# Kernel tuning notes

Measured on AMD Instinct MI355X. Metric: run time of the kernel, lower is better.

Reference implementation:

```python
import jax, jax.numpy as jnp
import numpy as np

NEG = -1.0e4  # finite stand-in for log(0) of the zero initial state (exp(NEG)==0 in fp32)


def log_g(x):
    # log of g(x) = where(x>=0, x+0.5, sigmoid(x))
    return jnp.where(x >= 0, jnp.log(jax.nn.relu(x) + 0.5), -jax.nn.softplus(-x))


def setup_inputs() -> dict:
    key = jax.random.key(0)
    k1, k2, k3 = jax.random.split(key, 3)
    B, S, D, H, O = 8, 8192, 512, 512, 512
    x = jax.random.normal(k1, (B, S, D), dtype=jnp.float32)
    is_init = jnp.zeros((B,), dtype=bool)  # unused in training mode (h_0 is None)
    W_hg = jax.random.normal(k2, (2 * H, D), dtype=jnp.float32) / np.float32(np.sqrt(D))
    W_out = jax.random.normal(k3, (O, H), dtype=jnp.float32) / np.float32(np.sqrt(H))
    return {"x": x, "is_init": is_init, "W_hg": W_hg, "W_out": W_out}


def reference(x, is_init, W_hg, W_out):
    B, S, _ = x.shape
    H = W_hg.shape[0] // 2
    hg = jnp.einsum('bsd,ed->bse', x, W_hg)          # [B,S,2H]
    hidden, gate = hg[..., :H], hg[..., H:]
    log_coeffs = -jax.nn.softplus(gate)              # log(1 - z)
    log_values = -jax.nn.softplus(-gate) + log_g(hidden)  # log z + log g(h~)
    # prepend h_0 = 0 -> log(h_0) ~ NEG; pad coeffs with a leading 0
    log_values = jnp.concatenate(
        [jnp.full((B, 1, H), NEG, dtype=x.dtype), log_values], axis=1)
    log_coeffs = jnp.pad(log_coeffs, ((0, 0), (1, 0), (0, 0)))
    # Heinsen log-space associative scan
    a_star = jnp.cumsum(log_coeffs, axis=1)
    log_h = a_star + jax.lax.cumlogsumexp(log_values - a_star, axis=1)
    h = jnp.exp(log_h)[:, 1:]                        # drop the h_0 slot -> [B,S,H]
    h_n = h[:, -1:]                                  # [B,1,H]
    out = jnp.einsum('bsh,oh->bso', h, W_out)        # [B,S,O]
    return (out, h_n)
```

## Files before the change

kernel.cpp:

```cpp
#include <hip/hip_runtime.h>
#include <stdint.h>

typedef __bf16 bf16;
typedef bf16 bf16x8 __attribute__((ext_vector_type(8)));
typedef bf16 bf16x4 __attribute__((ext_vector_type(4)));
typedef float f32x4 __attribute__((ext_vector_type(4)));

#define MFMA16(a, b, c) __builtin_amdgcn_mfma_f32_16x16x32_bf16(a, b, c, 0, 0, 0)

__device__ __forceinline__ void gll16(const void* g, void* l) {
    __builtin_amdgcn_global_load_lds(
        (const __attribute__((address_space(1))) void*)g,
        (__attribute__((address_space(3))) void*)l, 16, 0, 0);
}

__device__ __forceinline__ float frcp(float x) { return __builtin_amdgcn_rcpf(x); }

__device__ __forceinline__ float bflo(uint32_t u) {
    union { uint32_t i; float f; } x; x.i = u << 16; return x.f;
}
__device__ __forceinline__ float bfhi(uint32_t u) {
    union { uint32_t i; float f; } x; x.i = u & 0xffff0000u; return x.f;
}
__device__ __forceinline__ uint32_t packcv(float c, float v) {
    union { bf16 b[2]; uint32_t u; } p;
    p.b[0] = (bf16)c; p.b[1] = (bf16)v; return p.u;
}

__global__ __launch_bounds__(256) void conv_kernel(
    const float* __restrict__ X, const float* __restrict__ Whg,
    const float* __restrict__ Wout, bf16* __restrict__ Xbf,
    bf16* __restrict__ Whg_bf, bf16* __restrict__ Wout_bf) {
    int i = blockIdx.x * 256 + threadIdx.x;
    if (i < 8388608) {
        f32x4 v = ((const f32x4*)X)[i];
        ((bf16x4*)Xbf)[i] = __builtin_convertvector(v, bf16x4);
    } else if (i < 8388608 + 131072) {
        int j = i - 8388608;
        f32x4 v = ((const f32x4*)Whg)[j];
        ((bf16x4*)Whg_bf)[j] = __builtin_convertvector(v, bf16x4);
    } else {
        int j = i - (8388608 + 131072);
        f32x4 v = ((const f32x4*)Wout)[j];
        ((bf16x4*)Wout_bf)[j] = __builtin_convertvector(v, bf16x4);
    }
}

__global__ __launch_bounds__(256) void gemm1_kernel(
    const bf16* __restrict__ Xbf, const bf16* __restrict__ W,
    uint32_t* __restrict__ CV) {
    constexpr int K = 512;
    __shared__ bf16 As[128 * 64];
    __shared__ bf16 Bh[128 * 64];
    __shared__ bf16 Bg[128 * 64];

    const int t = threadIdx.x;
    const size_t m0 = (size_t)blockIdx.x * 128;
    const int n0 = blockIdx.y * 128;
    const int w = t >> 6, lane = t & 63;
    const int wm = (w >> 1) * 64, wn = (w & 1) * 64;
    const int r16 = lane & 15, quad = lane >> 4;
    const int sw = r16 & 7;

    f32x4 ah[4][4] = {};
    f32x4 ag[4][4] = {};

    for (int k0 = 0; k0 < K; k0 += 64) {
        __syncthreads();
        #pragma unroll
        for (int r = 0; r < 4; ++r) {
            int g = r * 256 + t;
            int row = g >> 3;
            int c8 = (g & 7) ^ (row & 7);
            gll16(Xbf + (m0 + row) * K + k0 + c8 * 8, &As[g * 8]);
            gll16(W + (size_t)(n0 + row) * K + k0 + c8 * 8, &Bh[g * 8]);
            gll16(W + (size_t)(512 + n0 + row) * K + k0 + c8 * 8, &Bg[g * 8]);
        }
        __syncthreads();
        #pragma unroll
        for (int kk = 0; kk < 2; ++kk) {
            const int kg = kk * 4 + quad;
            bf16x8 af[4], bhf[4], bgf[4];
            #pragma unroll
            for (int i = 0; i < 4; ++i) {
                int arow = wm + i * 16 + r16;
                af[i] = *(const bf16x8*)&As[arow * 64 + (kg ^ sw) * 8];
            }
            #pragma unroll
            for (int i = 0; i < 4; ++i) {
                int brow = wn + i * 16 + r16;
                bhf[i] = *(const bf16x8*)&Bh[brow * 64 + (kg ^ sw) * 8];
                bgf[i] = *(const bf16x8*)&Bg[brow * 64 + (kg ^ sw) * 8];
            }
            #pragma unroll
            for (int mi = 0; mi < 4; ++mi)
                #pragma unroll
                for (int ni = 0; ni < 4; ++ni) {
                    ah[mi][ni] = MFMA16(af[mi], bhf[ni], ah[mi][ni]);
                    ag[mi][ni] = MFMA16(af[mi], bgf[ni], ag[mi][ni]);
                }
        }
    }
    #pragma unroll
    for (int mi = 0; mi < 4; ++mi)
        #pragma unroll
        for (int ni = 0; ni < 4; ++ni)
            #pragma unroll
            for (int r = 0; r < 4; ++r) {
                size_t row = m0 + wm + mi * 16 + quad * 4 + r;
                int col = n0 + wn + ni * 16 + r16;
                float hid = ah[mi][ni][r], gat = ag[mi][ni][r];
                float z = frcp(1.f + __expf(-gat));
                float c = 1.f - z;
                float gv = hid >= 0.f ? hid + 0.5f : frcp(1.f + __expf(-hid));
                CV[row * 512 + col] = packcv(c, z * gv);
            }
}

#define NC 64
#define CHUNK 128

__global__ __launch_bounds__(256) void scan1_kernel(
    const uint32_t* __restrict__ CV, float2* __restrict__ agg) {
    int idx = blockIdx.x * 256 + threadIdx.x;
    int h = idx & 511;
    int ch = (idx >> 9) & (NC - 1);
    int b = idx >> 15;
    const uint32_t* p = CV + (((size_t)b * 8192 + (size_t)ch * CHUNK) * 512 + h);
    float C = 1.f, V = 0.f;
    for (int tt = 0; tt < CHUNK; tt += 8) {
        uint32_t u[8];
        #pragma unroll
        for (int j = 0; j < 8; ++j) u[j] = p[(size_t)(tt + j) * 512];
        #pragma unroll
        for (int j = 0; j < 8; ++j) {
            float c = bflo(u[j]), v = bfhi(u[j]);
            C *= c;
            V = c * V + v;
        }
    }
    agg[idx] = make_float2(C, V);
}

__global__ __launch_bounds__(256) void scan2_kernel(
    const float2* __restrict__ agg, float* __restrict__ h0) {
    int idx = blockIdx.x * 256 + threadIdx.x;
    int h = idx & 511;
    int b = idx >> 9;
    float hr = 0.f;
    for (int ch = 0; ch < NC; ++ch) {
        size_t o = ((size_t)b * NC + ch) * 512 + h;
        h0[o] = hr;
        float2 a = agg[o];
        hr = a.x * hr + a.y;
    }
}

__global__ __launch_bounds__(256) void scan3_kernel(
    const uint32_t* __restrict__ CV, const float* __restrict__ h0,
    bf16* __restrict__ Hbf, float* __restrict__ hn) {
    int idx = blockIdx.x * 256 + threadIdx.x;
    int h = idx & 511;
    int ch = (idx >> 9) & (NC - 1);
    int b = idx >> 15;
    size_t base = ((size_t)b * 8192 + (size_t)ch * CHUNK) * 512 + h;
    const uint32_t* p = CV + base;
    bf16* q = Hbf + base;
    float hcur = h0[idx];
    for (int tt = 0; tt < CHUNK; tt += 8) {
        uint32_t u[8];
        #pragma unroll
        for (int j = 0; j < 8; ++j) u[j] = p[(size_t)(tt + j) * 512];
        #pragma unroll
        for (int j = 0; j < 8; ++j) {
            float c = bflo(u[j]), v = bfhi(u[j]);
            hcur = c * hcur + v;
            q[(size_t)(tt + j) * 512] = (bf16)hcur;
        }
    }
    if (ch == NC - 1) hn[b * 512 + h] = hcur;
}

__global__ __launch_bounds__(256) void gemm2_kernel(
    const bf16* __restrict__ Ah, const bf16* __restrict__ Wo,
    float* __restrict__ Out) {
    constexpr int K = 512;
    __shared__ bf16 As[128 * 64];
    __shared__ bf16 Bs[128 * 64];
    const int t = threadIdx.x;
    const size_t m0 = (size_t)blockIdx.x * 128;
    const int n0 = blockIdx.y * 128;
    const int w = t >> 6, lane = t & 63;
    const int wm = (w >> 1) * 64, wn = (w & 1) * 64;
    const int r16 = lane & 15, quad = lane >> 4;
    const int sw = r16 & 7;
    f32x4 acc[4][4] = {};
    for (int k0 = 0; k0 < K; k0 += 64) {
        __syncthreads();
        #pragma unroll
        for (int r = 0; r < 4; ++r) {
            int g = r * 256 + t;
            int row = g >> 3;
            int c8 = (g & 7) ^ (row & 7);
            gll16(Ah + (m0 + row) * K + k0 + c8 * 8, &As[g * 8]);
            gll16(Wo + (size_t)(n0 + row) * K + k0 + c8 * 8, &Bs[g * 8]);
        }
        __syncthreads();
        #pragma unroll
        for (int kk = 0; kk < 2; ++kk) {
            const int kg = kk * 4 + quad;
            bf16x8 af[4], bf[4];
            #pragma unroll
            for (int i = 0; i < 4; ++i)
                af[i] = *(const bf16x8*)&As[(wm + i * 16 + r16) * 64 + (kg ^ sw) * 8];
            #pragma unroll
            for (int i = 0; i < 4; ++i)
                bf[i] = *(const bf16x8*)&Bs[(wn + i * 16 + r16) * 64 + (kg ^ sw) * 8];
            #pragma unroll
            for (int mi = 0; mi < 4; ++mi)
                #pragma unroll
                for (int ni = 0; ni < 4; ++ni)
                    acc[mi][ni] = MFMA16(af[mi], bf[ni], acc[mi][ni]);
        }
    }
    #pragma unroll
    for (int mi = 0; mi < 4; ++mi)
        #pragma unroll
        for (int ni = 0; ni < 4; ++ni)
            #pragma unroll
            for (int r = 0; r < 4; ++r) {
                size_t row = m0 + wm + mi * 16 + quad * 4 + r;
                int col = n0 + wn + ni * 16 + r16;
                Out[row * 512 + col] = acc[mi][ni][r];
            }
}

extern "C" void kernel_launch(void* const* d_in, const int* in_sizes, int n_in,
                              void* d_out, int out_size, void* d_ws, size_t ws_size,
                              hipStream_t stream) {
    const float* x    = (const float*)d_in[0];
    const float* Whg  = (const float*)d_in[2];
    const float* Wout = (const float*)d_in[3];
    float* out = (float*)d_out;

    const int M = 8 * 8192;

    char* ws = (char*)d_ws;
    bf16*     Xbf     = (bf16*)ws;
    bf16*     Hbf     = (bf16*)ws;
    bf16*     Whg_bf  = (bf16*)(ws + 67108864);
    bf16*     Wout_bf = (bf16*)(ws + 68157440);
    uint32_t* CV      = (uint32_t*)(ws + 68681728);
    float2*   agg     = (float2*)(ws + 202899456);
    float*    h0      = (float*)(ws + 204996608);

    conv_kernel<<<33536, 256, 0, stream>>>(x, Whg, Wout, Xbf, Whg_bf, Wout_bf);

    dim3 g1(M / 128, 4);
    gemm1_kernel<<<g1, 256, 0, stream>>>(Xbf, Whg_bf, CV);

    scan1_kernel<<<(8 * NC * 512) / 256, 256, 0, stream>>>(CV, agg);
    scan2_kernel<<<16, 256, 0, stream>>>(agg, h0);
    scan3_kernel<<<(8 * NC * 512) / 256, 256, 0, stream>>>(CV, h0, Hbf,
                                                           out + (size_t)M * 512);

    dim3 g2(M / 128, 4);
    gemm2_kernel<<<g2, 256, 0, stream>>>(Hbf, Wout_bf, out);
}
```

Before: 492.6 us.

## Double-buffer LDS and enlarge GEMM tiles to 256 rows with 8 waves

Both GEMM kernels now prefetch the next K-slice into a second LDS buffer while computing on the current one, waiting with partial vmcnt instead of a full sync. The M tile doubles to 256 rows with 512 threads per block, and MFMA sections are wrapped in raised wave priority. The aim is to hide global-to-LDS latency and improve reuse of the B tiles. In exchange, gemm1's LDS use grows to 128 KB per block, which may limit occupancy, and the hand-written vmcnt counts must match the number of loads issued per stage.

```diff
diff --git a/kernel.cpp b/kernel.cpp
--- a/kernel.cpp
+++ b/kernel.cpp
@@ -46,16 +46,16 @@
     }
 }
 
-__global__ __launch_bounds__(256) void gemm1_kernel(
+__global__ __launch_bounds__(512, 2) void gemm1_kernel(
     const bf16* __restrict__ Xbf, const bf16* __restrict__ W,
     uint32_t* __restrict__ CV) {
     constexpr int K = 512;
-    __shared__ bf16 As[128 * 64];
-    __shared__ bf16 Bh[128 * 64];
-    __shared__ bf16 Bg[128 * 64];
+    __shared__ bf16 As[2][256 * 64];
+    __shared__ bf16 Bh[2][128 * 64];
+    __shared__ bf16 Bg[2][128 * 64];
 
     const int t = threadIdx.x;
-    const size_t m0 = (size_t)blockIdx.x * 128;
+    const size_t m0 = (size_t)blockIdx.x * 256;
     const int n0 = blockIdx.y * 128;
     const int w = t >> 6, lane = t & 63;
     const int wm = (w >> 1) * 64, wn = (w & 1) * 64;
@@ -65,33 +65,49 @@
     f32x4 ah[4][4] = {};
     f32x4 ag[4][4] = {};
 
-    for (int k0 = 0; k0 < K; k0 += 64) {
-        __syncthreads();
+    auto stage = [&](int buf, int k0) {
         #pragma unroll
         for (int r = 0; r < 4; ++r) {
-            int g = r * 256 + t;
+            int g = r * 512 + t;
             int row = g >> 3;
             int c8 = (g & 7) ^ (row & 7);
-            gll16(Xbf + (m0 + row) * K + k0 + c8 * 8, &As[g * 8]);
-            gll16(W + (size_t)(n0 + row) * K + k0 + c8 * 8, &Bh[g * 8]);
-            gll16(W + (size_t)(512 + n0 + row) * K + k0 + c8 * 8, &Bg[g * 8]);
-        }
-        __syncthreads();
+            gll16(Xbf + (m0 + row) * K + k0 + c8 * 8, &As[buf][g * 8]);
+        }
+        #pragma unroll
+        for (int r = 0; r < 2; ++r) {
+            int g = r * 512 + t;
+            int row = g >> 3;
+            int c8 = (g & 7) ^ (row & 7);
+            gll16(W + (size_t)(n0 + row) * K + k0 + c8 * 8, &Bh[buf][g * 8]);
+            gll16(W + (size_t)(512 + n0 + row) * K + k0 + c8 * 8, &Bg[buf][g * 8]);
+        }
+    };
+
+    stage(0, 0);
+    #pragma unroll 2
+    for (int ks = 0; ks < 8; ++ks) {
+        const int cur = ks & 1;
+        if (ks < 7) {
+            stage(cur ^ 1, (ks + 1) * 64);
+            asm volatile("s_waitcnt vmcnt(8)" ::: "memory");
+        } else {
+            asm volatile("s_waitcnt vmcnt(0)" ::: "memory");
+        }
+        __builtin_amdgcn_s_barrier();
+        asm volatile("" ::: "memory");
         #pragma unroll
         for (int kk = 0; kk < 2; ++kk) {
             const int kg = kk * 4 + quad;
             bf16x8 af[4], bhf[4], bgf[4];
             #pragma unroll
+            for (int i = 0; i < 4; ++i)
+                af[i] = *(const bf16x8*)&As[cur][(wm + i * 16 + r16) * 64 + (kg ^ sw) * 8];
+            #pragma unroll
             for (int i = 0; i < 4; ++i) {
-                int arow = wm + i * 16 + r16;
-                af[i] = *(const bf16x8*)&As[arow * 64 + (kg ^ sw) * 8];
+                bhf[i] = *(const bf16x8*)&Bh[cur][(wn + i * 16 + r16) * 64 + (kg ^ sw) * 8];
+                bgf[i] = *(const bf16x8*)&Bg[cur][(wn + i * 16 + r16) * 64 + (kg ^ sw) * 8];
             }
-            #pragma unroll
-            for (int i = 0; i < 4; ++i) {
-                int brow = wn + i * 16 + r16;
-                bhf[i] = *(const bf16x8*)&Bh[brow * 64 + (kg ^ sw) * 8];
-                bgf[i] = *(const bf16x8*)&Bg[brow * 64 + (kg ^ sw) * 8];
-            }
+            __builtin_amdgcn_s_setprio(1);
             #pragma unroll
             for (int mi = 0; mi < 4; ++mi)
                 #pragma unroll
@@ -99,8 +115,12 @@
                     ah[mi][ni] = MFMA16(af[mi], bhf[ni], ah[mi][ni]);
                     ag[mi][ni] = MFMA16(af[mi], bgf[ni], ag[mi][ni]);
                 }
-        }
-    }
+            __builtin_amdgcn_s_setprio(0);
+        }
+        asm volatile("" ::: "memory");
+        __builtin_amdgcn_s_barrier();
+    }
+
     #pragma unroll
     for (int mi = 0; mi < 4; ++mi)
         #pragma unroll
@@ -181,47 +201,70 @@
     if (ch == NC - 1) hn[b * 512 + h] = hcur;
 }
 
-__global__ __launch_bounds__(256) void gemm2_kernel(
+__global__ __launch_bounds__(512, 2) void gemm2_kernel(
     const bf16* __restrict__ Ah, const bf16* __restrict__ Wo,
     float* __restrict__ Out) {
     constexpr int K = 512;
-    __shared__ bf16 As[128 * 64];
-    __shared__ bf16 Bs[128 * 64];
+    __shared__ bf16 As[2][256 * 64];
+    __shared__ bf16 Bs[2][128 * 64];
     const int t = threadIdx.x;
-    const size_t m0 = (size_t)blockIdx.x * 128;
+    const size_t m0 = (size_t)blockIdx.x * 256;
     const int n0 = blockIdx.y * 128;
     const int w = t >> 6, lane = t & 63;
     const int wm = (w >> 1) * 64, wn = (w & 1) * 64;
     const int r16 = lane & 15, quad = lane >> 4;
     const int sw = r16 & 7;
     f32x4 acc[4][4] = {};
-    for (int k0 = 0; k0 < K; k0 += 64) {
-        __syncthreads();
+
+    auto stage = [&](int buf, int k0) {
         #pragma unroll
         for (int r = 0; r < 4; ++r) {
-            int g = r * 256 + t;
+            int g = r * 512 + t;
             int row = g >> 3;
             int c8 = (g & 7) ^ (row & 7);
-            gll16(Ah + (m0 + row) * K + k0 + c8 * 8, &As[g * 8]);
-            gll16(Wo + (size_t)(n0 + row) * K + k0 + c8 * 8, &Bs[g * 8]);
-        }
-        __syncthreads();
+            gll16(Ah + (m0 + row) * K + k0 + c8 * 8, &As[buf][g * 8]);
+        }
+        #pragma unroll
+        for (int r = 0; r < 2; ++r) {
+            int g = r * 512 + t;
+            int row = g >> 3;
+            int c8 = (g & 7) ^ (row & 7);
+            gll16(Wo + (size_t)(n0 + row) * K + k0 + c8 * 8, &Bs[buf][g * 8]);
+        }
+    };
+
+    stage(0, 0);
+    #pragma unroll 2
+    for (int ks = 0; ks < 8; ++ks) {
+        const int cur = ks & 1;
+        if (ks < 7) {
+            stage(cur ^ 1, (ks + 1) * 64);
+            asm volatile("s_waitcnt vmcnt(6)" ::: "memory");
+        } else {
+            asm volatile("s_waitcnt vmcnt(0)" ::: "memory");
+        }
+        __builtin_amdgcn_s_barrier();
+        asm volatile("" ::: "memory");
         #pragma unroll
         for (int kk = 0; kk < 2; ++kk) {
             const int kg = kk * 4 + quad;
-            bf16x8 af[4], bf[4];
+            bf16x8 af[4], bff[4];
             #pragma unroll
             for (int i = 0; i < 4; ++i)
-                af[i] = *(const bf16x8*)&As[(wm + i * 16 + r16) * 64 + (kg ^ sw) * 8];
+                af[i] = *(const bf16x8*)&As[cur][(wm + i * 16 + r16) * 64 + (kg ^ sw) * 8];
             #pragma unroll
             for (int i = 0; i < 4; ++i)
-                bf[i] = *(const bf16x8*)&Bs[(wn + i * 16 + r16) * 64 + (kg ^ sw) * 8];
+                bff[i] = *(const bf16x8*)&Bs[cur][(wn + i * 16 + r16) * 64 + (kg ^ sw) * 8];
+            __builtin_amdgcn_s_setprio(1);
             #pragma unroll
             for (int mi = 0; mi < 4; ++mi)
                 #pragma unroll
                 for (int ni = 0; ni < 4; ++ni)
-                    acc[mi][ni] = MFMA16(af[mi], bf[ni], acc[mi][ni]);
-        }
+                    acc[mi][ni] = MFMA16(af[mi], bff[ni], acc[mi][ni]);
+            __builtin_amdgcn_s_setprio(0);
+        }
+        asm volatile("" ::: "memory");
+        __builtin_amdgcn_s_barrier();
     }
     #pragma unroll
     for (int mi = 0; mi < 4; ++mi)
@@ -256,14 +299,14 @@
 
     conv_kernel<<<33536, 256, 0, stream>>>(x, Whg, Wout, Xbf, Whg_bf, Wout_bf);
 
-    dim3 g1(M / 128, 4);
-    gemm1_kernel<<<g1, 256, 0, stream>>>(Xbf, Whg_bf, CV);
+    dim3 g1(M / 256, 4);
+    gemm1_kernel<<<g1, 512, 0, stream>>>(Xbf, Whg_bf, CV);
 
     scan1_kernel<<<(8 * NC * 512) / 256, 256, 0, stream>>>(CV, agg);
     scan2_kernel<<<16, 256, 0, stream>>>(agg, h0);
     scan3_kernel<<<(8 * NC * 512) / 256, 256, 0, stream>>>(CV, h0, Hbf,
                                                            out + (size_t)M * 512);
 
-    dim3 g2(M / 128, 4);
-    gemm2_kernel<<<g2, 256, 0, stream>>>(Hbf, Wout_bf, out);
-}
+    dim3 g2(M / 256, 4);
+    gemm2_kernel<<<g2, 512, 0, stream>>>(Hbf, Wout_bf, out);
+}
```

New measurement: 507.0 us. +2.9%, slower.
